# Kernel optimization log

Measured on AMD Instinct MI355X. Metric: run time of the kernel, lower is better.

Reference implementation:

```python
import jax, jax.numpy as jnp
import numpy as np

V = 32000; D = 128; L = 2048; B = 4
DI = 256; DS = 16; K = 4; H = 4; NM = 6; NA = 2; PAD = 0


def setup_inputs() -> dict:
    key = jax.random.key(0)
    ks = jax.random.split(key, 24)
    n = lambda i, shape, s: jax.random.normal(ks[i], shape, dtype=jnp.float32) * s
    inp = {}
    inp["input_ids"] = jax.random.randint(ks[0], (B, L), 0, V)
    inp["token_types"] = jax.random.randint(ks[1], (B, L), 0, 10)
    inp["timestamps"] = jax.random.uniform(ks[2], (B, L), dtype=jnp.float32)
    inp["emb"] = n(3, (V, D), 0.02).at[PAD].set(0.0)
    inp["type_emb"] = n(4, (10, D), 0.02)
    inp["te_freqs"] = n(5, (D // 2,), 0.1)
    inp["te_phases"] = jnp.zeros((D // 2,), jnp.float32)
    inp["te_w"] = n(6, (D, D), 0.05)
    inp["te_b"] = jnp.zeros((D,), jnp.float32)
    # Mamba blocks (stacked over NM)
    inp["m_norm_w"] = jnp.ones((NM, D), jnp.float32)
    inp["m_norm_b"] = jnp.zeros((NM, D), jnp.float32)
    inp["m_in_w"] = n(7, (NM, 2 * DI, D), 0.05)
    inp["m_conv_w"] = n(8, (NM, DI, 1, K), 0.2)   # depthwise, OIH with I=1
    inp["m_conv_b"] = jnp.zeros((NM, DI), jnp.float32)
    inp["m_dt_w"] = n(9, (NM, DI, DI), 0.05)
    inp["m_dt_b"] = jnp.zeros((NM, DI), jnp.float32)
    inp["m_B_w"] = n(10, (NM, DS, DI), 0.05)
    inp["m_C_w"] = n(11, (NM, DS, DI), 0.05)
    inp["m_D"] = jnp.ones((NM, DI), jnp.float32)
    inp["m_A_log"] = jnp.broadcast_to(jnp.log(jnp.arange(1, DS + 1, dtype=jnp.float32)), (NM, DI, DS)) + 0.0
    inp["m_out_w"] = n(12, (NM, D, DI), 0.05)
    # Attention blocks (stacked over NA)
    inp["a_ln1_w"] = jnp.ones((NA, D), jnp.float32)
    inp["a_ln1_b"] = jnp.zeros((NA, D), jnp.float32)
    inp["a_qkv_w"] = n(13, (NA, 3 * D, D), 0.05)
    inp["a_qkv_b"] = jnp.zeros((NA, 3 * D), jnp.float32)
    inp["a_out_w"] = n(14, (NA, D, D), 0.05)
    inp["a_out_b"] = jnp.zeros((NA, D), jnp.float32)
    inp["a_ln2_w"] = jnp.ones((NA, D), jnp.float32)
    inp["a_ln2_b"] = jnp.zeros((NA, D), jnp.float32)
    inp["a_f1_w"] = n(15, (NA, 4 * D, D), 0.05)
    inp["a_f1_b"] = jnp.zeros((NA, 4 * D), jnp.float32)
    inp["a_f2_w"] = n(16, (NA, D, 4 * D), 0.05)
    inp["a_f2_b"] = jnp.zeros((NA, D), jnp.float32)
    # Task head (n_tasks=1)
    inp["h_ln_w"] = jnp.ones((D,), jnp.float32)
    inp["h_ln_b"] = jnp.zeros((D,), jnp.float32)
    inp["h_w"] = n(17, (1, D), 0.05)
    inp["h_b"] = jnp.zeros((1,), jnp.float32)
    return inp


def _ln(x, w, b, eps=1e-5):
    mu = x.mean(-1, keepdims=True)
    var = ((x - mu) ** 2).mean(-1, keepdims=True)
    return (x - mu) * jax.lax.rsqrt(var + eps) * w + b


def _mamba(x, nw, nb, inw, cw, cb, dtw, dtb, bw, cpw, Dp, Alog, ow):
    res = x
    xn = _ln(x, nw, nb)
    xz = xn @ inw.T                              # [B,L,2*DI]
    xp, z = jnp.split(xz, 2, axis=-1)
    # causal depthwise conv: left-pad K-1, take first L outputs
    xc = jax.lax.conv_general_dilated(
        xp.transpose(0, 2, 1), cw, (1,), [(K - 1, 0)],
        feature_group_count=DI, dimension_numbers=("NCH", "OIH", "NCH"))
    xc = (xc + cb[None, :, None]).transpose(0, 2, 1)
    xc = jax.nn.silu(xc)
    dt = jax.nn.softplus(xc @ dtw.T + dtb)       # [B,L,DI]
    Bm = xc @ bw.T                               # [B,L,DS]
    Cm = xc @ cpw.T                              # [B,L,DS]
    A = -jnp.exp(Alog)                           # [DI,DS]

    def step(h, inp):
        dt_t, x_t, b_t, c_t = inp                # [B,DI],[B,DI],[B,DS],[B,DS]
        h = h * jnp.exp(A * dt_t[..., None]) + (x_t * dt_t)[..., None] * b_t[:, None, :]
        return h, (h * c_t[:, None, :]).sum(-1)

    xs = (jnp.moveaxis(dt, 1, 0), jnp.moveaxis(xc, 1, 0),
          jnp.moveaxis(Bm, 1, 0), jnp.moveaxis(Cm, 1, 0))
    h0 = jnp.zeros((x.shape[0], DI, DS), x.dtype)
    _, y = jax.lax.scan(step, h0, xs)            # y: [L,B,DI]
    y = jnp.moveaxis(y, 0, 1)
    y = y + xc * Dp
    y = y * jax.nn.silu(z)
    return res + y @ ow.T


def _attn(x, l1w, l1b, qkvw, qkvb, ow, ob, l2w, l2b, f1w, f1b, f2w, f2b):
    res = x
    xn = _ln(x, l1w, l1b)
    qkv = xn @ qkvw.T + qkvb
    q, k, v = jnp.split(qkv, 3, axis=-1)
    dh = D // H
    rs = lambda t: t.reshape(t.shape[0], t.shape[1], H, dh)
    q, k, v = rs(q), rs(k), rs(v)
    sc = jnp.einsum("bqhd,bkhd->bhqk", q, k) / jnp.sqrt(jnp.float32(dh))
    p = jax.nn.softmax(sc, axis=-1)
    o = jnp.einsum("bhqk,bkhd->bqhd", p, v).reshape(x.shape)
    x = res + o @ ow.T + ob
    ff = jax.nn.gelu(_ln(x, l2w, l2b) @ f1w.T + f1b, approximate=False) @ f2w.T + f2b
    return x + ff


def reference(input_ids, token_types, timestamps, emb, type_emb, te_freqs, te_phases, te_w, te_b,
              m_norm_w, m_norm_b, m_in_w, m_conv_w, m_conv_b, m_dt_w, m_dt_b, m_B_w, m_C_w,
              m_D, m_A_log, m_out_w,
              a_ln1_w, a_ln1_b, a_qkv_w, a_qkv_b, a_out_w, a_out_b, a_ln2_w, a_ln2_b,
              a_f1_w, a_f1_b, a_f2_w, a_f2_b, h_ln_w, h_ln_b, h_w, h_b):
    t = timestamps[..., None]
    enc = jnp.concatenate([jnp.sin(t * te_freqs + te_phases),
                           jnp.cos(t * te_freqs + te_phases)], axis=-1)
    x = emb[input_ids] + type_emb[token_types] + enc @ te_w.T + te_b
    attn_every = (NM + NA) // NA
    mi = 0; ai = 0
    for i in range(NM + NA):
        if (i + 1) % attn_every == 0:
            x = _attn(x, a_ln1_w[ai], a_ln1_b[ai], a_qkv_w[ai], a_qkv_b[ai],
                      a_out_w[ai], a_out_b[ai], a_ln2_w[ai], a_ln2_b[ai],
                      a_f1_w[ai], a_f1_b[ai], a_f2_w[ai], a_f2_b[ai])
            ai += 1
        else:
            x = _mamba(x, m_norm_w[mi], m_norm_b[mi], m_in_w[mi], m_conv_w[mi], m_conv_b[mi],
                       m_dt_w[mi], m_dt_b[mi], m_B_w[mi], m_C_w[mi], m_D[mi], m_A_log[mi], m_out_w[mi])
            mi += 1
    cls = x[:, 0, :]
    return (_ln(cls, h_ln_w, h_ln_b) @ h_w.T + h_b)[:, 0]
```

## Files before the change

kernel.cpp:

```cpp
#include <hip/hip_runtime.h>
#include <hip/hip_bf16.h>
#include <math.h>

constexpr int Ll = 2048, Bb = 4, DIi = 256, Hh = 4;
constexpr int TOK = Bb * Ll;
constexpr int NC = 128;
constexpr int CH = 16;
constexpr float LOG2E = 1.442695040888963f;

#define DEV __device__ __forceinline__

DEV float siluf(float v)     { return v / (1.f + expf(-v)); }
DEV float softplusf(float v) { return (v > 20.f) ? v : log1pf(expf(v)); }
DEV float geluf(float v)     { return 0.5f * v * (1.f + erff(v * 0.7071067811865476f)); }

#if defined(__has_builtin)
#if __has_builtin(__builtin_amdgcn_exp2f)
#define EXP2F __builtin_amdgcn_exp2f
#endif
#endif
#ifndef EXP2F
#define EXP2F exp2f
#endif

DEV short f2bf(float f) {
    union { float f; unsigned u; } a; a.f = f;
    unsigned r = (a.u + 0x7fffu + ((a.u >> 16) & 1u)) >> 16;
    return (short)r;
}

using bf16x8 = __attribute__((ext_vector_type(8))) short;
using f16x8  = __attribute__((ext_vector_type(8))) _Float16;
using f32x4  = __attribute__((ext_vector_type(4))) float;

__global__ __launch_bounds__(256) void wprep_kernel(
    const float* s0, const float* s1, const float* s2, const float* s3,
    const float* s4, const float* s5, const float* s6, const float* s7,
    const float* s8, const float* s9, _Float16* dst)
{
    constexpr int base[10] = {0, 16384, 409600, 802816, 827392, 851968,
                              1048576, 1146880, 1179648, 1310720};
    constexpr int nseg[10] = {16384, 393216, 393216, 24576, 24576, 196608,
                              98304, 32768, 131072, 131072};
    int seg = blockIdx.y;
    int t = blockIdx.x * 256 + threadIdx.x;
    if (t >= nseg[seg]) return;
    const float* src;
    switch (seg) {
        case 0: src = s0; break; case 1: src = s1; break;
        case 2: src = s2; break; case 3: src = s3; break;
        case 4: src = s4; break; case 5: src = s5; break;
        case 6: src = s6; break; case 7: src = s7; break;
        case 8: src = s8; break; default: src = s9; break;
    }
    dst[base[seg] + t] = (_Float16)src[t];
}

__global__ __launch_bounds__(256) void gather_enc_kernel(
    const int* __restrict__ ids, const int* __restrict__ tts,
    const float* __restrict__ ts, const float* __restrict__ emb,
    const float* __restrict__ temb, const float* __restrict__ freqs,
    const float* __restrict__ phases, float* __restrict__ x,
    float* __restrict__ enc)
{
    int tok = blockIdx.x * 2 + (threadIdx.x >> 7);
    int d = threadIdx.x & 127;
    float tval = ts[tok];
    int j = d & 63;
    float a = tval * freqs[j] + phases[j];
    enc[(size_t)tok * 128 + d] = (d < 64) ? sinf(a) : cosf(a);
    int id = ids[tok];
    int tt = tts[tok];
    x[(size_t)tok * 128 + d] = emb[(size_t)id * 128 + d] + temb[(size_t)tt * 128 + d];
}

__global__ __launch_bounds__(256) void ln_stats_kernel(
    const float* __restrict__ x, float2* __restrict__ stats)
{
    int wid = threadIdx.x >> 6, lane = threadIdx.x & 63;
    int tok = blockIdx.x * 4 + wid;
    float2 v = *(const float2*)(x + (size_t)tok * 128 + lane * 2);
    float s = v.x + v.y, sq = v.x * v.x + v.y * v.y;
#pragma unroll
    for (int o = 32; o > 0; o >>= 1) { s += __shfl_xor(s, o); sq += __shfl_xor(sq, o); }
    if (lane == 0) {
        float mu = s * (1.f / 128.f);
        float var = sq * (1.f / 128.f) - mu * mu;
        stats[tok] = make_float2(mu, rsqrtf(var + 1e-5f));
    }
}

template <int ACT, bool BIAS, bool ADD, bool LNA, int MODE>
__global__ __launch_bounds__(256) void gemm64_kernel(
    const float* __restrict__ A, const _Float16* __restrict__ W,
    const float* __restrict__ bias, float* __restrict__ C,
    const float* __restrict__ lnw, const float* __restrict__ lnb,
    const float2* __restrict__ stats,
    const _Float16* __restrict__ Bw, const _Float16* __restrict__ Cw,
    float* __restrict__ bmo, float* __restrict__ cmo,
    short* __restrict__ kbf, short* __restrict__ vbf,
    int M, int N, int Kd, int lda, int ldc)
{
    __shared__ _Float16 As[64][72];
    __shared__ _Float16 Ws[64][72];
    const int by = blockIdx.y;
    const bool isBC = (MODE == 1) && (by == (int)gridDim.y - 1);
    const int bm0 = blockIdx.x * 64, bn0 = by * 64;
    const int tid = threadIdx.x;
    const int w = tid >> 6, l = tid & 63;
    const int wr = w >> 1, wc = w & 1;
    const int fr = l & 15, fk = (l >> 4) * 8;
    const int srow = tid >> 2, skc = (tid & 3) * 16;
    float mu = 0.f, rstd = 1.f;
    if (LNA) { float2 st = stats[bm0 + srow]; mu = st.x; rstd = st.y; }
    f32x4 acc[2][2] = {};

    for (int k0 = 0; k0 < Kd; k0 += 64) {
        const float* ap = A + (size_t)(bm0 + srow) * lda + k0 + skc;
        const _Float16* wp;
        if (isBC) {
            if (srow < 16)      wp = Bw + (size_t)srow * Kd + k0 + skc;
            else if (srow < 32) wp = Cw + (size_t)(srow - 16) * Kd + k0 + skc;
            else                wp = Bw + k0 + skc;
        } else {
            wp = W + (size_t)(bn0 + srow) * Kd + k0 + skc;
        }
        float af[16];
#pragma unroll
        for (int q = 0; q < 4; q++)
            *(float4*)(af + q * 4) = *(const float4*)(ap + q * 4);
        f16x8 wb0 = *(const f16x8*)wp;
        f16x8 wb1 = *(const f16x8*)(wp + 8);
        if (LNA) {
#pragma unroll
            for (int q = 0; q < 4; q++) {
                float4 w4 = *(const float4*)(lnw + k0 + skc + q * 4);
                float4 b4 = *(const float4*)(lnb + k0 + skc + q * 4);
                af[q*4+0] = (af[q*4+0] - mu) * rstd * w4.x + b4.x;
                af[q*4+1] = (af[q*4+1] - mu) * rstd * w4.y + b4.y;
                af[q*4+2] = (af[q*4+2] - mu) * rstd * w4.z + b4.z;
                af[q*4+3] = (af[q*4+3] - mu) * rstd * w4.w + b4.w;
            }
        }
        f16x8 ab0, ab1;
#pragma unroll
        for (int q = 0; q < 8; q++) {
            ab0[q] = (_Float16)af[q]; ab1[q] = (_Float16)af[q + 8];
        }
        __syncthreads();
        *(f16x8*)&As[srow][skc]     = ab0;
        *(f16x8*)&As[srow][skc + 8] = ab1;
        *(f16x8*)&Ws[srow][skc]     = wb0;
        *(f16x8*)&Ws[srow][skc + 8] = wb1;
        __syncthreads();
#pragma unroll
        for (int ks = 0; ks < 64; ks += 32) {
            f16x8 afr0 = *(const f16x8*)&As[wr * 32 + fr][ks + fk];
            f16x8 afr1 = *(const f16x8*)&As[wr * 32 + 16 + fr][ks + fk];
            f16x8 wfr0 = *(const f16x8*)&Ws[wc * 32 + fr][ks + fk];
            f16x8 wfr1 = *(const f16x8*)&Ws[wc * 32 + 16 + fr][ks + fk];
            acc[0][0] = __builtin_amdgcn_mfma_f32_16x16x32_f16(afr0, wfr0, acc[0][0], 0, 0, 0);
            acc[0][1] = __builtin_amdgcn_mfma_f32_16x16x32_f16(afr0, wfr1, acc[0][1], 0, 0, 0);
            acc[1][0] = __builtin_amdgcn_mfma_f32_16x16x32_f16(afr1, wfr0, acc[1][0], 0, 0, 0);
            acc[1][1] = __builtin_amdgcn_mfma_f32_16x16x32_f16(afr1, wfr1, acc[1][1], 0, 0, 0);
        }
    }
#pragma unroll
    for (int ri = 0; ri < 2; ri++)
#pragma unroll
    for (int ci = 0; ci < 2; ci++) {
        const int lcol = wc * 32 + ci * 16 + fr;
        const int col = bn0 + lcol;
        const int row0 = bm0 + wr * 32 + ri * 16 + (l >> 4) * 4;
        if (isBC) {
            if (lcol < 32) {
                float* dst = (lcol < 16) ? bmo : cmo;
                const int cc = lcol & 15;
#pragma unroll
                for (int r = 0; r < 4; r++)
                    dst[(size_t)(row0 + r) * 16 + cc] = acc[ri][ci][r];
            }
        } else if (MODE == 2) {
            const float bv = bias[col];
            const int b = row0 >> 11, tl0 = row0 & 2047;
            if (col < 128) {
#pragma unroll
                for (int r = 0; r < 4; r++)
                    C[(size_t)(row0 + r) * 128 + col] = acc[ri][ci][r] + bv;
            } else if (col < 256) {
                const int hc = col - 128;
                short* kp = kbf + ((size_t)(b * 4 + (hc >> 5)) * 2048 + tl0) * 32 + (hc & 31);
#pragma unroll
                for (int r = 0; r < 4; r++)
                    kp[(size_t)r * 32] = f2bf(acc[ri][ci][r] + bv);
            } else {
                const int hc = col - 256;
                short4 vk;
#pragma unroll
                for (int r = 0; r < 4; r++)
                    ((short*)&vk)[r] = f2bf(acc[ri][ci][r] + bv);
                *(short4*)(vbf + ((size_t)(b * 4 + (hc >> 5)) * 32 + (hc & 31)) * 2048 + tl0) = vk;
            }
        } else {
            const float bv = BIAS ? bias[col] : 0.f;
#pragma unroll
            for (int r = 0; r < 4; r++) {
                float t = acc[ri][ci][r] + bv;
                if (ACT == 1) t = softplusf(t);
                if (ACT == 2) t = geluf(t);
                float* p = C + (size_t)(row0 + r) * ldc + col;
                if (ADD) t += *p;
                *p = t;
            }
        }
    }
}

__global__ __launch_bounds__(256) void conv_kernel(
    const float* __restrict__ xz, const float* __restrict__ cw,
    const float* __restrict__ cb, float* __restrict__ xc)
{
    int g = blockIdx.x * 256 + threadIdx.x;
    int c = g & 255;
    int t = (g >> 8) & 2047;
    int b = g >> 19;
    float4 w4 = *(const float4*)(cw + (size_t)c * 4);
    float acc = cb[c];
    const float* base = xz + ((size_t)b * 2048 + t) * 512 + c;
    if (t >= 3) {
        acc += base[-3 * 512] * w4.x + base[-2 * 512] * w4.y + base[-512] * w4.z + base[0] * w4.w;
    } else {
        const float wv[4] = {w4.x, w4.y, w4.z, w4.w};
#pragma unroll
        for (int kk = 0; kk < 4; kk++) {
            int tt = t - 3 + kk;
            if (tt >= 0) acc += xz[((size_t)b * 2048 + tt) * 512 + c] * wv[kk];
        }
    }
    xc[g] = siluf(acc);
}

__global__ __launch_bounds__(256) void scan1_kernel(
    const float* __restrict__ dt, const float* __restrict__ xc,
    const float* __restrict__ bm, const float* __restrict__ Alog,
    float* __restrict__ F, float* __restrict__ sumdt)
{
    int c = threadIdx.x;
    int k = blockIdx.x & (NC - 1);
    int b = blockIdx.x / NC;
    __shared__ float sB[CH][16];
    int t0 = k * CH;
    if (threadIdx.x < CH * 4) {
        int r = threadIdx.x >> 2, c4 = (threadIdx.x & 3) << 2;
        *(float4*)&sB[r][c4] = *(const float4*)(bm + ((size_t)b * 2048 + t0 + r) * 16 + c4);
    }
    float A2[16];
#pragma unroll
    for (int s = 0; s < 16; s++) A2[s] = -expf(Alog[(size_t)c * 16 + s]) * LOG2E;
    __syncthreads();
    float h[16] = {};
    float sd = 0.f;
    size_t base = ((size_t)b * 2048 + t0) * 256 + c;
    for (int tt = 0; tt < CH; tt++) {
        float d  = dt[base + (size_t)tt * 256];
        float xv = xc[base + (size_t)tt * 256];
        sd += d;
        float xdt = xv * d;
#pragma unroll
        for (int s = 0; s < 16; s++) h[s] = h[s] * EXP2F(A2[s] * d) + xdt * sB[tt][s];
    }
    size_t fo = (((size_t)b * NC + k) * 256 + c) * 16;
#pragma unroll
    for (int s = 0; s < 16; s += 4) *(float4*)(F + fo + s) = make_float4(h[s], h[s+1], h[s+2], h[s+3]);
    sumdt[((size_t)b * NC + k) * 256 + c] = sd;
}

__global__ __launch_bounds__(256) void scan2_kernel(
    float* __restrict__ F, const float* __restrict__ sumdt,
    const float* __restrict__ Alog)
{
    int g = blockIdx.x * 256 + threadIdx.x;
    int s = g & 15, c = (g >> 4) & 255, b = g >> 12;
    float A2 = -expf(Alog[(size_t)c * 16 + s]) * LOG2E;
    float h = 0.f;
    for (int k = 0; k < NC; k++) {
        size_t o = (((size_t)b * NC + k) * 256 + c) * 16 + s;
        float tmp = F[o];
        F[o] = h;
        h = h * EXP2F(A2 * sumdt[((size_t)b * NC + k) * 256 + c]) + tmp;
    }
}

__global__ __launch_bounds__(256) void scan3_kernel(
    const float* __restrict__ dt, const float* __restrict__ xc,
    const float* __restrict__ bm, const float* __restrict__ cm,
    const float* __restrict__ xz, const float* __restrict__ Alog,
    const float* __restrict__ Dp, const float* __restrict__ Hs,
    float* __restrict__ y)
{
    int c = threadIdx.x;
    int k = blockIdx.x & (NC - 1);
    int b = blockIdx.x / NC;
    __shared__ float sB[CH][16], sC[CH][16];
    int t0 = k * CH;
    if (threadIdx.x < CH * 4) {
        int r = threadIdx.x >> 2, c4 = (threadIdx.x & 3) << 2;
        *(float4*)&sB[r][c4] = *(const float4*)(bm + ((size_t)b * 2048 + t0 + r) * 16 + c4);
        *(float4*)&sC[r][c4] = *(const float4*)(cm + ((size_t)b * 2048 + t0 + r) * 16 + c4);
    }
    float A2[16];
#pragma unroll
    for (int s = 0; s < 16; s++) A2[s] = -expf(Alog[(size_t)c * 16 + s]) * LOG2E;
    __syncthreads();
    float h[16];
    size_t ho = (((size_t)b * NC + k) * 256 + c) * 16;
#pragma unroll
    for (int s = 0; s < 16; s++) h[s] = Hs[ho + s];
    float Dv = Dp[c];
    size_t base  = ((size_t)b * 2048 + t0) * 256 + c;
    size_t zbase = ((size_t)b * 2048 + t0) * 512 + 256 + c;
    for (int tt = 0; tt < CH; tt++) {
        float d  = dt[base + (size_t)tt * 256];
        float xv = xc[base + (size_t)tt * 256];
        float xdt = xv * d;
        float yv = 0.f;
#pragma unroll
        for (int s = 0; s < 16; s++) {
            h[s] = h[s] * EXP2F(A2[s] * d) + xdt * sB[tt][s];
            yv += h[s] * sC[tt][s];
        }
        yv += xv * Dv;
        float zv = xz[zbase + (size_t)tt * 512];
        y[base + (size_t)tt * 256] = yv * siluf(zv);
    }
}

__global__ __launch_bounds__(256) void attn_part_kernel(
    const float* __restrict__ qbuf, const short* __restrict__ kbf,
    const short* __restrict__ vbf, float* __restrict__ pO, float* __restrict__ pml)
{
    __shared__ short Pt[4][64][18];
    const int qt = blockIdx.x, b = blockIdx.z;
    const int h = blockIdx.y >> 2, sp = blockIdx.y & 3;
    const int tid = threadIdx.x;
    const int w = tid >> 6, l = tid & 63;
    const int q16 = l & 15, g = l >> 4;
    const float cQ = 0.25503634043f;

    const int qrow = qt * 64 + w * 16 + q16;
    const float* qp = qbuf + ((size_t)(b * 2048 + qrow)) * 128 + 32 * h + g * 8;
    bf16x8 qfrag;
    {
        float qf[8];
        *(float4*)qf       = *(const float4*)qp;
        *(float4*)(qf + 4) = *(const float4*)(qp + 4);
#pragma unroll
        for (int i = 0; i < 8; i++) qfrag[i] = f2bf(qf[i] * cQ);
    }
    const int bh = b * 4 + h;
    const short* kb = kbf + ((size_t)bh * 2048) * 32;
    const short* vb = vbf + ((size_t)bh * 32) * 2048;

    float m = -1e30f, lsum = 0.f;
    f32x4 O0 = {0.f, 0.f, 0.f, 0.f}, O1 = {0.f, 0.f, 0.f, 0.f};
    const f32x4 zf = {0.f, 0.f, 0.f, 0.f};

    auto ldKV = [&](bf16x8 (&kf)[4], bf16x8 (&vf)[4], int t) {
#pragma unroll
        for (int kt = 0; kt < 4; kt++)
            kf[kt] = *(const bf16x8*)(kb + (size_t)(t * 64 + kt * 16 + q16) * 32 + g * 8);
#pragma unroll
        for (int c = 0; c < 2; c++)
#pragma unroll
            for (int hf = 0; hf < 2; hf++)
                vf[c * 2 + hf] = *(const bf16x8*)(vb + (size_t)(q16 + 16 * hf) * 2048 + t * 64 + 32 * c + g * 8);
    };

    auto step = [&](bf16x8 (&kf)[4], bf16x8 (&vf)[4]) {
        f32x4 St[4];
#pragma unroll
        for (int kt = 0; kt < 4; kt++)
            St[kt] = __builtin_amdgcn_mfma_f32_16x16x32_bf16(kf[kt], qfrag, zf, 0, 0, 0);
        float pm = St[0][0];
#pragma unroll
        for (int kt = 0; kt < 4; kt++)
#pragma unroll
            for (int r = 0; r < 4; r++) pm = fmaxf(pm, St[kt][r]);
        pm = fmaxf(pm, __shfl_xor(pm, 16));
        pm = fmaxf(pm, __shfl_xor(pm, 32));
        float mn = fmaxf(m, pm);
        float rs = EXP2F(m - mn);
        float ps = 0.f;
#pragma unroll
        for (int kt = 0; kt < 4; kt++)
#pragma unroll
            for (int r = 0; r < 4; r++) {
                float p = EXP2F(St[kt][r] - mn);
                ps += p;
                Pt[w][kt * 16 + g * 4 + r][q16] = f2bf(p);
            }
        ps += __shfl_xor(ps, 16);
        ps += __shfl_xor(ps, 32);
        lsum = lsum * rs + ps;
        m = mn;
        O0 *= rs; O1 *= rs;
#pragma unroll
        for (int c = 0; c < 2; c++) {
            bf16x8 pb;
#pragma unroll
            for (int i = 0; i < 8; i++) pb[i] = Pt[w][c * 32 + g * 8 + i][q16];
            O0 = __builtin_amdgcn_mfma_f32_16x16x32_bf16(vf[c * 2 + 0], pb, O0, 0, 0, 0);
            O1 = __builtin_amdgcn_mfma_f32_16x16x32_bf16(vf[c * 2 + 1], pb, O1, 0, 0, 0);
        }
    };

    const int ts0 = sp * 8;
    bf16x8 kA[4], kB[4], vA[4], vB[4];
    ldKV(kA, vA, ts0);
    for (int t = ts0; t < ts0 + 8; t += 2) {
        if (t + 1 < ts0 + 8) ldKV(kB, vB, t + 1);
        step(kA, vA);
        if (t + 2 < ts0 + 8) ldKV(kA, vA, t + 2);
        step(kB, vB);
    }

    size_t po = (((size_t)(bh * 4 + sp)) * 2048 + qrow) * 32;
#pragma unroll
    for (int r = 0; r < 4; r++) {
        pO[po + g * 4 + r]      = O0[r];
        pO[po + 16 + g * 4 + r] = O1[r];
    }
    if (g == 0) {
        size_t mo = (((size_t)(bh * 4 + sp)) * 2048 + qrow) * 2;
        pml[mo]     = m;
        pml[mo + 1] = lsum;
    }
}

__global__ __launch_bounds__(256) void attn_comb_kernel(
    const float* __restrict__ pO, const float* __restrict__ pml,
    float* __restrict__ aout)
{
    int gid = blockIdx.x * 256 + threadIdx.x;
    int d = gid & 31, q = (gid >> 5) & 2047, bh = gid >> 16;
    float m[4], lv[4], M = -1e30f;
#pragma unroll
    for (int s = 0; s < 4; s++) {
        size_t mo = (((size_t)(bh * 4 + s)) * 2048 + q) * 2;
        m[s] = pml[mo]; lv[s] = pml[mo + 1];
        M = fmaxf(M, m[s]);
    }
    float L = 0.f, o = 0.f;
#pragma unroll
    for (int s = 0; s < 4; s++) {
        float wgt = EXP2F(m[s] - M);
        L += lv[s] * wgt;
        o += pO[(((size_t)(bh * 4 + s)) * 2048 + q) * 32 + d] * wgt;
    }
    int b = bh >> 2, h = bh & 3;
    aout[((size_t)(b * 2048 + q)) * 128 + h * 32 + d] = o / L;
}

__global__ __launch_bounds__(128) void head_kernel(
    const float* __restrict__ x, const float* __restrict__ w,
    const float* __restrict__ bsp, const float* __restrict__ hw,
    const float* __restrict__ hb, float* __restrict__ out)
{
    int bb = blockIdx.x;
    int d = threadIdx.x;
    int wid = d >> 6, lane = d & 63;
    float v = x[(size_t)bb * 2048 * 128 + d];
    float s = v, sq = v * v;
#pragma unroll
    for (int o = 32; o > 0; o >>= 1) { s += __shfl_xor(s, o); sq += __shfl_xor(sq, o); }
    __shared__ float red[4];
    if (lane == 0) { red[wid] = s; red[2 + wid] = sq; }
    __syncthreads();
    s = red[0] + red[1]; sq = red[2] + red[3];
    float mu = s * (1.f / 128.f);
    float var = sq * (1.f / 128.f) - mu * mu;
    float xn = (v - mu) * rsqrtf(var + 1e-5f) * w[d] + bsp[d];
    float pr = xn * hw[d];
#pragma unroll
    for (int o = 32; o > 0; o >>= 1) pr += __shfl_xor(pr, o);
    __syncthreads();
    if (lane == 0) red[wid] = pr;
    __syncthreads();
    if (d == 0) out[bb] = red[0] + red[1] + hb[0];
}

constexpr size_t OFF_X  = 0;
constexpr size_t OFF_XZ = (size_t)1 << 20;
constexpr size_t OFF_XC = (size_t)5 << 20;
constexpr size_t OFF_DT = (size_t)7 << 20;
constexpr size_t OFF_Y  = (size_t)9 << 20;
constexpr size_t OFF_BM = (size_t)11 << 20;
constexpr size_t OFF_CM = OFF_BM + 131072;
constexpr size_t OFF_SD = OFF_CM + 131072;
constexpr size_t OFF_ST = OFF_SD + 131072;
constexpr size_t OFF_F  = OFF_ST + 16384;
constexpr size_t OFF_WF = OFF_F + ((size_t)2 << 20);
constexpr size_t WS_FLOATS = OFF_WF + 720896;

extern "C" void kernel_launch(void* const* d_in, const int* in_sizes, int n_in,
                              void* d_out, int out_size, void* d_ws, size_t ws_size,
                              hipStream_t stream)
{
    const int*   ids   = (const int*)d_in[0];
    const int*   tts   = (const int*)d_in[1];
    const float* tstmp = (const float*)d_in[2];
    const float* emb   = (const float*)d_in[3];
    const float* temb  = (const float*)d_in[4];
    const float* tef   = (const float*)d_in[5];
    const float* tep   = (const float*)d_in[6];
    const float* tew   = (const float*)d_in[7];
    const float* tebi  = (const float*)d_in[8];
    const float* mnw   = (const float*)d_in[9];
    const float* mnb   = (const float*)d_in[10];
    const float* minw  = (const float*)d_in[11];
    const float* mcwp  = (const float*)d_in[12];
    const float* mcb   = (const float*)d_in[13];
    const float* mdtw  = (const float*)d_in[14];
    const float* mdtb  = (const float*)d_in[15];
    const float* mbw   = (const float*)d_in[16];
    const float* mcw2  = (const float*)d_in[17];
    const float* mD    = (const float*)d_in[18];
    const float* mAl   = (const float*)d_in[19];
    const float* mow   = (const float*)d_in[20];
    const float* al1w  = (const float*)d_in[21];
    const float* al1b  = (const float*)d_in[22];
    const float* aqkvw = (const float*)d_in[23];
    const float* aqkvb = (const float*)d_in[24];
    const float* aow   = (const float*)d_in[25];
    const float* aob   = (const float*)d_in[26];
    const float* al2w  = (const float*)d_in[27];
    const float* al2b  = (const float*)d_in[28];
    const float* af1w  = (const float*)d_in[29];
    const float* af1b  = (const float*)d_in[30];
    const float* af2w  = (const float*)d_in[31];
    const float* af2b  = (const float*)d_in[32];
    const float* hlnw  = (const float*)d_in[33];
    const float* hlnb  = (const float*)d_in[34];
    const float* hw    = (const float*)d_in[35];
    const float* hb    = (const float*)d_in[36];
    float* out = (float*)d_out;
    float* wsf = (float*)d_ws;
    if (ws_size < WS_FLOATS * sizeof(float)) return;

    float* x    = wsf + OFF_X;
    float* xz   = wsf + OFF_XZ;
    float* xc   = wsf + OFF_XC;
    float* dtb  = wsf + OFF_DT;
    float* yb   = wsf + OFF_Y;
    float* bm   = wsf + OFF_BM;
    float* cm   = wsf + OFF_CM;
    float* sdb  = wsf + OFF_SD;
    float2* stats = (float2*)(wsf + OFF_ST);
    float* Fb   = wsf + OFF_F;
    float* ff   = xz;
    float* aout = yb;
    float* qbuf = xc;
    float* pO   = xz;
    float* pml  = dtb;
    float* encb = Fb;
    short* kbf  = (short*)(wsf + OFF_F);
    short* vbf  = (short*)(wsf + OFF_F + ((size_t)1 << 20));
    _Float16* wf16 = (_Float16*)(wsf + OFF_WF);

    const _Float16* tew16   = wf16;
    const _Float16* minw16  = wf16 + 16384;
    const _Float16* mdtw16  = wf16 + 409600;
    const _Float16* mbw16   = wf16 + 802816;
    const _Float16* mcw216  = wf16 + 827392;
    const _Float16* mow16   = wf16 + 851968;
    const _Float16* aqkvw16 = wf16 + 1048576;
    const _Float16* aow16   = wf16 + 1146880;
    const _Float16* af1w16  = wf16 + 1179648;
    const _Float16* af2w16  = wf16 + 1310720;

    wprep_kernel<<<dim3(1536, 10), 256, 0, stream>>>(
        tew, minw, mdtw, mbw, mcw2, mow, aqkvw, aow, af1w, af2w, wf16);

    gather_enc_kernel<<<TOK / 2, 256, 0, stream>>>(ids, tts, tstmp, emb, temb, tef, tep, x, encb);
    gemm64_kernel<0, true, true, false, 0><<<dim3(128, 2), 256, 0, stream>>>(
        encb, tew16, tebi, x, nullptr, nullptr, nullptr, nullptr, nullptr,
        nullptr, nullptr, nullptr, nullptr, TOK, 128, 128, 128, 128);

    int mi = 0, ai = 0;
    for (int i = 0; i < 8; i++) {
        if ((i + 1) % 4 == 0) {
            ln_stats_kernel<<<TOK / 4, 256, 0, stream>>>(x, stats);
            gemm64_kernel<0, true, false, true, 2><<<dim3(128, 6), 256, 0, stream>>>(
                x, aqkvw16 + (size_t)ai * 49152, aqkvb + ai * 384, qbuf,
                al1w + ai * 128, al1b + ai * 128, stats, nullptr, nullptr,
                nullptr, nullptr, kbf, vbf, TOK, 384, 128, 128, 128);
            attn_part_kernel<<<dim3(32, 16, Bb), 256, 0, stream>>>(qbuf, kbf, vbf, pO, pml);
            attn_comb_kernel<<<4096, 256, 0, stream>>>(pO, pml, aout);
            gemm64_kernel<0, true, true, false, 0><<<dim3(128, 2), 256, 0, stream>>>(
                aout, aow16 + (size_t)ai * 16384, aob + ai * 128, x,
                nullptr, nullptr, nullptr, nullptr, nullptr,
                nullptr, nullptr, nullptr, nullptr, TOK, 128, 128, 128, 128);
            ln_stats_kernel<<<TOK / 4, 256, 0, stream>>>(x, stats);
            gemm64_kernel<2, true, false, true, 0><<<dim3(128, 8), 256, 0, stream>>>(
                x, af1w16 + (size_t)ai * 65536, af1b + ai * 512, ff,
                al2w + ai * 128, al2b + ai * 128, stats, nullptr, nullptr,
                nullptr, nullptr, nullptr, nullptr, TOK, 512, 128, 128, 512);
            gemm64_kernel<0, true, true, false, 0><<<dim3(128, 2), 256, 0, stream>>>(
                ff, af2w16 + (size_t)ai * 65536, af2b + ai * 128, x,
                nullptr, nullptr, nullptr, nullptr, nullptr,
                nullptr, nullptr, nullptr, nullptr, TOK, 128, 512, 512, 128);
            ai++;
        } else {
            const float* Al = mAl + (size_t)mi * DIi * 16;
            ln_stats_kernel<<<TOK / 4, 256, 0, stream>>>(x, stats);
            gemm64_kernel<0, false, false, true, 0><<<dim3(128, 8), 256, 0, stream>>>(
                x, minw16 + (size_t)mi * 65536, nullptr, xz,
                mnw + mi * 128, mnb + mi * 128, stats, nullptr, nullptr,
                nullptr, nullptr, nullptr, nullptr, TOK, 512, 128, 128, 512);
            conv_kernel<<<8192, 256, 0, stream>>>(xz, mcwp + (size_t)mi * DIi * 4, mcb + mi * DIi, xc);
            gemm64_kernel<1, true, false, false, 1><<<dim3(128, 5), 256, 0, stream>>>(
                xc, mdtw16 + (size_t)mi * 65536, mdtb + mi * 256, dtb,
                nullptr, nullptr, nullptr,
                mbw16 + (size_t)mi * 4096, mcw216 + (size_t)mi * 4096,
                bm, cm, nullptr, nullptr, TOK, 256, 256, 256, 256);
            scan1_kernel<<<Bb * NC, 256, 0, stream>>>(dtb, xc, bm, Al, Fb, sdb);
            scan2_kernel<<<64, 256, 0, stream>>>(Fb, sdb, Al);
            scan3_kernel<<<Bb * NC, 256, 0, stream>>>(dtb, xc, bm, cm, xz, Al, mD + mi * 256, Fb, yb);
            gemm64_kernel<0, false, true, false, 0><<<dim3(128, 2), 256, 0, stream>>>(
                yb, mow16 + (size_t)mi * 32768, nullptr, x,
                nullptr, nullptr, nullptr, nullptr, nullptr,
                nullptr, nullptr, nullptr, nullptr, TOK, 128, 256, 256, 128);
            mi++;
        }
    }
    head_kernel<<<Bb, 128, 0, stream>>>(x, hlnw, hlnb, hw, hb, out);
}
```

Baseline: 732.1 us.

## Stage K/V tiles through double-buffered swizzled LDS in attention partial kernel

```diff
diff --git a/kernel.cpp b/kernel.cpp
--- a/kernel.cpp
+++ b/kernel.cpp
@@ -339,6 +339,8 @@
     const float* __restrict__ qbuf, const short* __restrict__ kbf,
     const short* __restrict__ vbf, float* __restrict__ pO, float* __restrict__ pml)
 {
+    __shared__ short Klds[2][64 * 32];
+    __shared__ short Vlds[2][32 * 64];
     __shared__ short Pt[4][64][18];
     const int qt = blockIdx.x, b = blockIdx.z;
     const int h = blockIdx.y >> 2, sp = blockIdx.y & 3;
@@ -361,22 +363,29 @@
     const short* kb = kbf + ((size_t)bh * 2048) * 32;
     const short* vb = vbf + ((size_t)bh * 32) * 2048;
 
+    const int vrow = tid >> 3;
+    const int vsw  = ((tid & 7) * 16) ^ ((vrow & 7) << 4);
+    const int ts0 = sp * 8;
+
+    bf16x8 kst, vst;
+    auto ldregs = [&](int t) {
+        kst = *(const bf16x8*)(kb + (size_t)t * 2048 + tid * 8);
+        vst = *(const bf16x8*)(vb + (size_t)vrow * 2048 + t * 64 + (vsw >> 1));
+    };
+    auto dswrite = [&](int buf) {
+        *(bf16x8*)&Klds[buf][tid * 8] = kst;
+        *(bf16x8*)&Vlds[buf][tid * 8] = vst;
+    };
+
     float m = -1e30f, lsum = 0.f;
     f32x4 O0 = {0.f, 0.f, 0.f, 0.f}, O1 = {0.f, 0.f, 0.f, 0.f};
     const f32x4 zf = {0.f, 0.f, 0.f, 0.f};
 
-    auto ldKV = [&](bf16x8 (&kf)[4], bf16x8 (&vf)[4], int t) {
+    auto step = [&](int buf) {
+        bf16x8 kf[4];
 #pragma unroll
         for (int kt = 0; kt < 4; kt++)
-            kf[kt] = *(const bf16x8*)(kb + (size_t)(t * 64 + kt * 16 + q16) * 32 + g * 8);
-#pragma unroll
-        for (int c = 0; c < 2; c++)
-#pragma unroll
-            for (int hf = 0; hf < 2; hf++)
-                vf[c * 2 + hf] = *(const bf16x8*)(vb + (size_t)(q16 + 16 * hf) * 2048 + t * 64 + 32 * c + g * 8);
-    };
-
-    auto step = [&](bf16x8 (&kf)[4], bf16x8 (&vf)[4]) {
+            kf[kt] = *(const bf16x8*)&Klds[buf][(kt * 16 + q16) * 32 + g * 8];
         f32x4 St[4];
 #pragma unroll
         for (int kt = 0; kt < 4; kt++)
@@ -409,19 +418,28 @@
             bf16x8 pb;
 #pragma unroll
             for (int i = 0; i < 8; i++) pb[i] = Pt[w][c * 32 + g * 8 + i][q16];
-            O0 = __builtin_amdgcn_mfma_f32_16x16x32_bf16(vf[c * 2 + 0], pb, O0, 0, 0, 0);
-            O1 = __builtin_amdgcn_mfma_f32_16x16x32_bf16(vf[c * 2 + 1], pb, O1, 0, 0, 0);
+#pragma unroll
+            for (int hf = 0; hf < 2; hf++) {
+                const int d = q16 + 16 * hf;
+                bf16x8 vf = *(const bf16x8*)&Vlds[buf][d * 64 + ((c * 32 + g * 8) ^ ((d & 7) << 3))];
+                if (hf == 0) O0 = __builtin_amdgcn_mfma_f32_16x16x32_bf16(vf, pb, O0, 0, 0, 0);
+                else         O1 = __builtin_amdgcn_mfma_f32_16x16x32_bf16(vf, pb, O1, 0, 0, 0);
+            }
         }
     };
 
-    const int ts0 = sp * 8;
-    bf16x8 kA[4], kB[4], vA[4], vB[4];
-    ldKV(kA, vA, ts0);
-    for (int t = ts0; t < ts0 + 8; t += 2) {
-        if (t + 1 < ts0 + 8) ldKV(kB, vB, t + 1);
-        step(kA, vA);
-        if (t + 2 < ts0 + 8) ldKV(kA, vA, t + 2);
-        step(kB, vB);
+    ldregs(ts0);
+    dswrite(0);
+    ldregs(ts0 + 1);
+    int cur = 0;
+    for (int i = 0; i < 8; i++) {
+        __syncthreads();
+        if (i + 1 < 8) {
+            dswrite(cur ^ 1);
+            if (i + 2 < 8) ldregs(ts0 + i + 2);
+        }
+        step(cur);
+        cur ^= 1;
     }
 
     size_t po = (((size_t)(bh * 4 + sp)) * 2048 + qrow) * 32;
```

Result: faster. 695.0 us (-5.1%).
